# Kernel tuning notes

Hardware: AMD Instinct MI355X
Metric: run time of the kernel (lower is better)

## Reference

```python
import jax, jax.numpy as jnp
import numpy as np

NB = 8          # num_bins
HID = 128       # hidden channels of coupling ResidualNet
TB = 3.0        # tail_bound
MINB = 1e-3     # min bin width / height
MIND = 1e-3     # min derivative
DCONST = float(np.log(np.exp(1.0 - MIND) - 1.0))  # softplus(DCONST)+MIND == 1
LU_EPS = 1e-3


def rqs_inverse(x, uw, uh, ud):
    """Inverse monotonic rational-quadratic spline with linear tails (nflows math).
    x: [B,F]; uw,uh broadcastable to [B,F,NB]; ud broadcastable to [B,F,NB-1]."""
    K = NB
    uw = jnp.broadcast_to(uw, x.shape + (K,))
    uh = jnp.broadcast_to(uh, x.shape + (K,))
    ud = jnp.broadcast_to(ud, x.shape + (K - 1,))
    ud = jnp.pad(ud, [(0, 0)] * x.ndim + [(1, 1)], constant_values=DCONST)  # boundary derivs = 1
    inside = (x >= -TB) & (x <= TB)
    xi = jnp.clip(x, -TB, TB)

    def knots(u):
        v = MINB + (1.0 - MINB * K) * jax.nn.softmax(u, -1)
        c = jnp.concatenate([jnp.zeros(x.shape + (1,), x.dtype), jnp.cumsum(v, -1)], -1)
        c = 2.0 * TB * c - TB
        c = c.at[..., 0].set(-TB).at[..., -1].set(TB)
        return c, c[..., 1:] - c[..., :-1]

    cw, w = knots(uw)   # x-knots / bin widths
    ch, h = knots(uh)   # y-knots / bin heights
    d = MIND + jax.nn.softplus(ud)  # [B,F,K+1] knot derivatives

    # searchsorted on cumheights (inverse direction)
    locs = ch.at[..., -1].add(1e-6)
    idx = jnp.clip(jnp.sum((xi[..., None] >= locs).astype(jnp.int32), -1) - 1, 0, K - 1)[..., None]
    g = lambda a: jnp.take_along_axis(a, idx, -1)[..., 0]
    in_cw, in_w, in_ch, in_h = g(cw), g(w), g(ch), g(h)
    delta = in_h / in_w
    d0 = g(d)
    d1 = jnp.take_along_axis(d, idx + 1, -1)[..., 0]

    t = xi - in_ch
    s = d0 + d1 - 2.0 * delta
    a = t * s + in_h * (delta - d0)
    b = in_h * d0 - t * s
    c = -delta * t
    root = (2.0 * c) / (-b - jnp.sqrt(b * b - 4.0 * a * c))
    out = root * in_w + in_cw
    tm = root * (1.0 - root)
    den = delta + s * tm
    dnum = delta ** 2 * (d1 * root ** 2 + 2.0 * delta * tm + d0 * (1.0 - root) ** 2)
    ld = -(jnp.log(dnum) - 2.0 * jnp.log(den))
    return jnp.where(inside, out, x), jnp.where(inside, ld, 0.0)


def resnet(x, Wi, bi, Wb, bb, Wo, bo):
    # nflows ResidualNet: initial linear, 2 pre-activation residual blocks, final linear
    t = x @ Wi + bi
    for j in range(2):
        r = jax.nn.relu(t) @ Wb[2 * j] + bb[2 * j]
        r = jax.nn.relu(r) @ Wb[2 * j + 1] + bb[2 * j + 1]
        t = t + r
    return t @ Wo + bo


def coupling_inverse(z, Wi, bi, Wb, bb, Wo, bo, uw_u, uh_u, ud_u):
    # alternating mask: even dims = identity split, odd dims = transform split
    ident, trans = z[:, 0::2], z[:, 1::2]
    # unconditional spline on identity features is inverted FIRST, then feeds the net
    ident, ld_u = rqs_inverse(ident, uw_u, uh_u, ud_u)
    B, F = trans.shape
    p = resnet(ident, Wi, bi, Wb, bb, Wo, bo).reshape(B, F, 3 * NB - 1)
    scale = 1.0 / np.sqrt(HID)  # nflows divides widths/heights by sqrt(hidden_features)
    trans, ld_t = rqs_inverse(trans, p[..., :NB] * scale, p[..., NB:2 * NB] * scale, p[..., 2 * NB:])
    out = jnp.stack([ident, trans], -1).reshape(B, -1)
    return out, jnp.sum(ld_u, -1) + jnp.sum(ld_t, -1)


def log_prob(x, loc, log_scale, Wi, bi, Wb, bb, Wo, bo, uw_u, uh_u, ud_u,
             lu_lower, lu_upper, lu_ud, lu_b, perms):
    N, T, D = x.shape
    z = x.reshape(-1, D)
    lq = jnp.zeros((z.shape[0],), x.dtype)
    for i in (2, 1, 0):  # flows = [C0,LU0,C1,LU1,C2,LU2]; invert in reverse order
        # LULinearPermute.inverse: permute, then y = L(Ux) + b, logdet = sum log diag(U)
        zp = z[:, perms[i]]
        diag = jax.nn.softplus(lu_ud[i]) + LU_EPS
        U = jnp.triu(lu_upper[i], 1) + jnp.diag(diag)
        L = jnp.tril(lu_lower[i], -1) + jnp.eye(D, dtype=x.dtype)
        z = (zp @ U.T) @ L.T + lu_b[i]
        lq = lq + jnp.sum(jnp.log(diag))
        z, ld = coupling_inverse(z, Wi[i], bi[i], Wb[i], bb[i], Wo[i], bo[i],
                                 uw_u[i], uh_u[i], ud_u[i])
        lq = lq + ld
    # DiagGaussian base log-prob
    lq = lq - 0.5 * D * jnp.log(2.0 * jnp.pi) \
            - jnp.sum(log_scale + 0.5 * ((z - loc) / jnp.exp(log_scale)) ** 2, -1)
    return lq.reshape(N, T)


def setup_inputs():
    key = jax.random.key(0)
    ks = jax.random.split(key, 16)
    N, T, D, F = 8, 512, 550, 275
    OUT = F * (3 * NB - 1)
    s = 0.1
    return {
        "x": jax.random.normal(ks[0], (N, T, D), jnp.float32),
        "loc": 0.1 * jax.random.normal(ks[1], (D,), jnp.float32),
        "log_scale": jnp.zeros((D,), jnp.float32),
        "Wi": s * jax.random.normal(ks[2], (3, F, HID), jnp.float32),
        "bi": jnp.zeros((3, HID), jnp.float32),
        "Wb": s * jax.random.normal(ks[3], (3, 4, HID, HID), jnp.float32),
        "bb": jnp.zeros((3, 4, HID), jnp.float32),
        "Wo": 0.01 * jax.random.normal(ks[4], (3, HID, OUT), jnp.float32),
        "bo": 0.01 * jax.random.normal(ks[5], (3, OUT), jnp.float32),
        "uw_u": jax.random.uniform(ks[6], (3, F, NB), jnp.float32),
        "uh_u": jax.random.uniform(ks[7], (3, F, NB), jnp.float32),
        "ud_u": jax.random.uniform(ks[8], (3, F, NB - 1), jnp.float32),
        "lu_lower": 0.05 * jax.random.normal(ks[9], (3, D, D), jnp.float32),
        "lu_upper": 0.05 * jax.random.normal(ks[10], (3, D, D), jnp.float32),
        "lu_ud": jnp.full((3, D), DCONST, jnp.float32),
        "lu_b": jnp.zeros((3, D), jnp.float32),
        "perms": jnp.stack([jax.random.permutation(ks[11 + i], D) for i in range(3)]).astype(jnp.int32),
    }


def reference(x, loc, log_scale, Wi, bi, Wb, bb, Wo, bo, uw_u, uh_u, ud_u,
              lu_lower, lu_upper, lu_ud, lu_b, perms):
    # log_prob(x).reshape(N, T); calculate_likelihood would just apply exp/nan->0/clamp on top.
    return log_prob(x, loc, log_scale, Wi, bi, Wb, bb, Wo, bo, uw_u, uh_u, ud_u,
                    lu_lower, lu_upper, lu_ud, lu_b, perms)
```

## Files before the change

kernel.cpp:

```cpp
#include <hip/hip_runtime.h>


#define D_DIM 550
#define D_PAD 576
#define N_PAD_A 640
#define F_DIM 275
#define F_PAD 320
#define FP_HALF 288
#define HID_DIM 128
#define OUT_DIM 6325
#define OUT_PAD 6400
#define FT_PAD 276
#define WO2_ROWS (FT_PAD*32)
#define WO_GX (WO2_ROWS/64)
#define B_ROWS 4096
#define NBINS 8
#define TB_C 3.0f
#define MINB_C 0.001f
#define MIND_C 0.001f
#define DCONST_C 0.53974233f
#define LUEPS_C 0.001f
#define RSQRT_HID 0.08838834764831845f

typedef unsigned short ushort_t;
typedef __attribute__((ext_vector_type(8))) short short8;
typedef __attribute__((ext_vector_type(8))) unsigned short ushort8;
typedef __attribute__((ext_vector_type(4))) float f32x4;

__device__ __forceinline__ ushort_t f2bf(float f){
    union{float f; unsigned u;} v; v.f = f;
    unsigned r = v.u + 0x7fffu + ((v.u>>16)&1u);
    return (ushort_t)(r>>16);
}
__device__ __forceinline__ float bf2f(ushort_t h){
    union{unsigned u; float f;} v; v.u = ((unsigned)h)<<16;
    return v.f;
}
__device__ __forceinline__ float softplusf(float x){
    return fmaxf(x, 0.f) + __logf(1.f + __expf(-fabsf(x)));
}

__device__ __forceinline__ void knots_from_u(const float* u, float* c, float* w){
    float m = u[0];
#pragma unroll
    for(int k=1;k<NBINS;k++) m = fmaxf(m, u[k]);
    float e[NBINS]; float s = 0.f;
#pragma unroll
    for(int k=0;k<NBINS;k++){ e[k] = __expf(u[k]-m); s += e[k]; }
    float inv = 1.f/s;
    float cum = 0.f;
    c[0] = -TB_C;
#pragma unroll
    for(int k=0;k<NBINS;k++){
        float v = MINB_C + (1.f - MINB_C*(float)NBINS)*e[k]*inv;
        cum += v;
        c[k+1] = 2.f*TB_C*cum - TB_C;
    }
    c[NBINS] = TB_C;
#pragma unroll
    for(int k=0;k<NBINS;k++) w[k] = c[k+1]-c[k];
}

__device__ __forceinline__ void rqs_inv(float x,
                                        const float* cw, const float* w,
                                        const float* ch, const float* h,
                                        const float* d,
                                        float& out, float& ld){
    bool inside = (x >= -TB_C) && (x <= TB_C);
    float xi = fminf(fmaxf(x, -TB_C), TB_C);
    int idx = 0;
#pragma unroll
    for(int j=1;j<NBINS;j++) idx += (xi >= ch[j]) ? 1 : 0;
    float icw=cw[0], iw=w[0], ich=ch[0], ih=h[0], d0=d[0], d1=d[1];
#pragma unroll
    for(int j=1;j<NBINS;j++){
        if(idx==j){ icw=cw[j]; iw=w[j]; ich=ch[j]; ih=h[j]; d0=d[j]; d1=d[j+1]; }
    }
    float delta = ih/iw;
    float t  = xi - ich;
    float s  = d0 + d1 - 2.f*delta;
    float a  = t*s + ih*(delta - d0);
    float b  = ih*d0 - t*s;
    float c  = -delta*t;
    float disc = b*b - 4.f*a*c;
    float root = 2.f*c / (-b - sqrtf(fmaxf(disc, 0.f)));
    float o  = root*iw + icw;
    float tm = root*(1.f-root);
    float den  = delta + s*tm;
    float dnum = delta*delta*(d1*root*root + 2.f*delta*tm + d0*(1.f-root)*(1.f-root));
    float l = 2.f*__logf(den) - __logf(dnum);
    out = inside ? o : x;
    ld  = inside ? l : 0.f;
}


__global__ void build_knots_kernel(const float* __restrict__ uw_u,
                                   const float* __restrict__ uh_u,
                                   const float* __restrict__ ud_u,
                                   float* __restrict__ knots){
    int g = blockIdx.x*blockDim.x + threadIdx.x;
    if(g >= 3*F_DIM) return;
    float* kb = knots + (size_t)g*43;
    float c[9], w[8];
    knots_from_u(uw_u + (size_t)g*8, c, w);
#pragma unroll
    for(int k=0;k<9;k++) kb[k]=c[k];
#pragma unroll
    for(int k=0;k<8;k++) kb[9+k]=w[k];
    knots_from_u(uh_u + (size_t)g*8, c, w);
#pragma unroll
    for(int k=0;k<9;k++) kb[17+k]=c[k];
#pragma unroll
    for(int k=0;k<8;k++) kb[26+k]=w[k];
    float dend = MIND_C + softplusf(DCONST_C);
    kb[34]=dend; kb[42]=dend;
    const float* ud = ud_u + (size_t)g*7;
#pragma unroll
    for(int k=0;k<7;k++) kb[35+k] = MIND_C + softplusf(ud[k]);
}

__global__ void logdiag_kernel(const float* __restrict__ lu_ud, float* __restrict__ outv){
    int tid = threadIdx.x;
    float s = 0.f;
    for(int k=tid; k<3*D_DIM; k+=256) s += __logf(softplusf(lu_ud[k]) + LUEPS_C);
#pragma unroll
    for(int o=32;o>0;o>>=1) s += __shfl_down(s, o);
    __shared__ float sm[4];
    if((tid&63)==0) sm[tid>>6]=s;
    __syncthreads();
    if(tid==0) outv[0] = sm[0]+sm[1]+sm[2]+sm[3];
}

__global__ void build_L_bf16(const float* __restrict__ lower,
                             ushort_t* __restrict__ Lmb){
    int l = blockIdx.z;
    lower += (size_t)l*D_DIM*D_DIM;
    Lmb += (size_t)l*N_PAD_A*D_PAD;
    int k = blockIdx.x*blockDim.x + threadIdx.x;
    int j = blockIdx.y;
    if(k >= D_DIM) return;
    float lv = (j>k) ? lower[(size_t)j*D_DIM+k] : (j==k ? 1.f : 0.f);
    Lmb[(size_t)j*D_PAD+k] = f2bf(lv);
}

__global__ void build_UT_bf16(const float* __restrict__ upper,
                              const float* __restrict__ ud,
                              const int* __restrict__ perm,
                              ushort_t* __restrict__ UpTb){
    int l = blockIdx.z;
    upper += (size_t)l*D_DIM*D_DIM; ud += (size_t)l*D_DIM; perm += (size_t)l*D_DIM;
    UpTb += (size_t)l*N_PAD_A*D_PAD;
    __shared__ float t[32][33];
    int j0 = blockIdx.x*32, k0 = blockIdx.y*32;
    int tx = threadIdx.x, ty = threadIdx.y;
#pragma unroll
    for(int i=0;i<32;i+=8){
        int j = j0+ty+i, k = k0+tx;
        float uv = 0.f;
        if(j<D_DIM && k<D_DIM){
            if(j<k)       uv = upper[(size_t)j*D_DIM+k];
            else if(j==k) uv = softplusf(ud[k]) + LUEPS_C;
        }
        t[ty+i][tx] = uv;
    }
    __syncthreads();
#pragma unroll
    for(int i=0;i<32;i+=8){
        int k = k0+ty+i, j = j0+tx;
        if(k<D_DIM)
            UpTb[(size_t)perm[k]*D_PAD + j] = f2bf(t[tx][ty+i]);
    }
}

__global__ void convert_pad(const float* __restrict__ in, ushort_t* __restrict__ out,
                            int M, int K, int Mpad, int Kpad){
    int idx = blockIdx.x*256 + threadIdx.x;
    if(idx >= Mpad*Kpad) return;
    int r = idx / Kpad, c = idx - r*Kpad;
    float v = (r<M && c<K) ? in[(size_t)r*K+c] : 0.f;
    out[idx] = f2bf(v);
}

template<int REMAP>
__global__ void transpose_convert(const float* __restrict__ in, ushort_t* __restrict__ out,
                                  int K, int N, int Kpad, int Npad, long s_in, long s_out){
    in += (size_t)blockIdx.z*s_in; out += (size_t)blockIdx.z*s_out;
    __shared__ float t[32][33];
    int kb = blockIdx.x*32, nb = blockIdx.y*32;
    int tx = threadIdx.x, ty = threadIdx.y;
#pragma unroll
    for(int i=0;i<32;i+=8){
        int k = kb+ty+i, n = nb+tx;
        t[ty+i][tx] = (k<K && n<N) ? in[(size_t)k*N+n] : 0.f;
    }
    __syncthreads();
#pragma unroll
    for(int i=0;i<32;i+=8){
        int n = nb+ty+i, k = kb+tx;
        if(REMAP){
            if(n < OUT_DIM && k < Kpad){
                int f = n/23, j = n - 23*f;
                out[(size_t)(f*32+j)*Kpad+k] = f2bf(t[tx][ty+i]);
            }
        } else if(n<Npad && k<Kpad){
            out[(size_t)n*Kpad+k] = f2bf(t[tx][ty+i]);
        }
    }
}

__global__ void reorder_bias(const float* __restrict__ bo, float* __restrict__ bo2){
    int idx = blockIdx.x*256 + threadIdx.x;
    if(idx >= 3*OUT_DIM) return;
    int l = idx/OUT_DIM, n = idx%OUT_DIM;
    int f = n/23, j = n - 23*f;
    bo2[(size_t)l*WO2_ROWS + f*32 + j] = bo[idx];
}

template<int OUTBF>
__global__ __launch_bounds__(256)
void gemm_mfma(const ushort_t* __restrict__ A, const ushort_t* __restrict__ Bt,
               const float* __restrict__ bias, void* __restrict__ Cv,
               int M, int N, int Kpad, long sA, long sB, long sC){
    A  += (size_t)blockIdx.z*sA;
    Bt += (size_t)blockIdx.z*sB;
    __shared__ ushort_t As[128][72];
    __shared__ ushort_t Bs[128][72];
    int tid = threadIdx.x;
    int row0 = blockIdx.y*128, col0 = blockIdx.x*128;
    int wave = tid>>6, lane = tid&63;
    int wm = wave&1, wn = wave>>1;
    int lm = lane&15, quad = lane>>4;
    f32x4 acc[4][4] = {};
    for(int k0=0; k0<Kpad; k0+=64){
#pragma unroll
        for(int it=0; it<4; it++){
            int c = tid + it*256;
            int r = c>>3, c8 = (c&7)*8;
            *(ushort8*)&As[r][c8] = *(const ushort8*)(A + (size_t)(row0+r)*Kpad + k0 + c8);
            *(ushort8*)&Bs[r][c8] = *(const ushort8*)(Bt + (size_t)(col0+r)*Kpad + k0 + c8);
        }
        __syncthreads();
#pragma unroll
        for(int ks=0; ks<2; ks++){
            short8 af[4], bfr[4];
#pragma unroll
            for(int i=0;i<4;i++){
                af[i]  = *(const short8*)&As[wm*64 + i*16 + lm][ks*32 + quad*8];
                bfr[i] = *(const short8*)&Bs[wn*64 + i*16 + lm][ks*32 + quad*8];
            }
#pragma unroll
            for(int i=0;i<4;i++)
#pragma unroll
                for(int j=0;j<4;j++)
                    acc[i][j] = __builtin_amdgcn_mfma_f32_16x16x32_bf16(af[i], bfr[j], acc[i][j], 0, 0, 0);
        }
        __syncthreads();
    }
#pragma unroll
    for(int i=0;i<4;i++){
        int rbase = row0 + wm*64 + i*16 + quad*4;
#pragma unroll
        for(int j=0;j<4;j++){
            int gc = col0 + wn*64 + j*16 + lm;
            if(gc >= N) continue;
            float bv = bias[gc];
#pragma unroll
            for(int r=0;r<4;r++){
                int gr = rbase + r;
                float v = acc[i][j][r] + bv;
                if(OUTBF) ((ushort_t*)Cv + (size_t)blockIdx.z*sC)[(size_t)gr*N+gc] = f2bf(v);
                else      ((float*)Cv + (size_t)blockIdx.z*sC)[(size_t)gr*N+gc] = v;
            }
        }
    }
}

__global__ __launch_bounds__(256)
void resnet_fused(const ushort_t* __restrict__ identb,
                  const ushort_t* __restrict__ WiT,
                  const float* __restrict__ bi,
                  const ushort_t* __restrict__ WbT,
                  const float* __restrict__ bb,
                  ushort_t* __restrict__ tb){
    __shared__ ushort_t As2[16][136];
    int tid = threadIdx.x, wave = tid>>6, lane = tid&63;
    int lm = lane&15, quad = lane>>4;
    int r0 = blockIdx.x*16;
    int arow = r0 + lm;
    f32x4 cur[2] = {};
    f32x4 tsv[2];
    for(int k0=0; k0<F_PAD; k0+=64){
        const ushort_t* ap = identb + (size_t)arow*F_PAD + k0 + quad*8;
        short8 af0 = *(const short8*)(ap);
        short8 af1 = *(const short8*)(ap + 32);
#pragma unroll
        for(int jj=0;jj<2;jj++){
            int n = (wave*2+jj)*16 + lm;
            const ushort_t* wp = WiT + (size_t)n*F_PAD + k0 + quad*8;
            short8 b0 = *(const short8*)(wp);
            short8 b1 = *(const short8*)(wp + 32);
            cur[jj] = __builtin_amdgcn_mfma_f32_16x16x32_bf16(af0, b0, cur[jj], 0, 0, 0);
            cur[jj] = __builtin_amdgcn_mfma_f32_16x16x32_bf16(af1, b1, cur[jj], 0, 0, 0);
        }
    }
#pragma unroll
    for(int jj=0;jj<2;jj++){
        float bv = bi[(wave*2+jj)*16 + lm];
#pragma unroll
        for(int r=0;r<4;r++) cur[jj][r] += bv;
        tsv[jj] = cur[jj];
    }
    short8 wA[2][4], wB[2][4];
#pragma unroll
    for(int jj=0;jj<2;jj++){
        int n = (wave*2+jj)*16 + lm;
        const ushort_t* wp = WbT + (size_t)n*128 + quad*8;
#pragma unroll
        for(int ks=0;ks<4;ks++) wA[jj][ks] = *(const short8*)(wp + ks*32);
    }
#pragma unroll
    for(int st=0; st<4; st++){
        __syncthreads();
#pragma unroll
        for(int jj=0;jj<2;jj++)
#pragma unroll
            for(int r=0;r<4;r++)
                As2[quad*4 + r][(wave*2+jj)*16 + lm] = f2bf(fmaxf(cur[jj][r], 0.f));
        if(st < 3){
#pragma unroll
            for(int jj=0;jj<2;jj++){
                int n = (wave*2+jj)*16 + lm;
                const ushort_t* wp = WbT + (size_t)(st+1)*128*128 + (size_t)n*128 + quad*8;
#pragma unroll
                for(int ks=0;ks<4;ks++){
                    if(st & 1) wA[jj][ks] = *(const short8*)(wp + ks*32);
                    else       wB[jj][ks] = *(const short8*)(wp + ks*32);
                }
            }
        }
        __syncthreads();
        short8 af[4];
#pragma unroll
        for(int ks=0;ks<4;ks++) af[ks] = *(const short8*)&As2[lm][ks*32 + quad*8];
        f32x4 acc[2] = {};
#pragma unroll
        for(int ks=0;ks<4;ks++){
#pragma unroll
            for(int jj=0;jj<2;jj++){
                short8 bf = (st & 1) ? wB[jj][ks] : wA[jj][ks];
                acc[jj] = __builtin_amdgcn_mfma_f32_16x16x32_bf16(af[ks], bf, acc[jj], 0, 0, 0);
            }
        }
#pragma unroll
        for(int jj=0;jj<2;jj++){
            float bv = bb[st*128 + (wave*2+jj)*16 + lm];
#pragma unroll
            for(int r=0;r<4;r++) acc[jj][r] += bv;
        }
        if(st==1 || st==3){
#pragma unroll
            for(int jj=0;jj<2;jj++){
#pragma unroll
                for(int r=0;r<4;r++) acc[jj][r] += tsv[jj][r];
                tsv[jj] = acc[jj];
            }
        }
#pragma unroll
        for(int jj=0;jj<2;jj++) cur[jj] = acc[jj];
    }
#pragma unroll
    for(int jj=0;jj<2;jj++)
#pragma unroll
        for(int r=0;r<4;r++)
            tb[(size_t)(r0 + quad*4 + r)*HID_DIM + (wave*2+jj)*16 + lm] = f2bf(cur[jj][r]);
}

__global__ __launch_bounds__(256)
void zodd_transpose(const float* __restrict__ z2, float* __restrict__ z2oddT){
    __shared__ float s[32][65];
    int r0 = blockIdx.x*64, f0 = blockIdx.y*32;
    int tid = threadIdx.x;
    int f = tid & 31, rb = tid >> 5;
#pragma unroll
    for(int rr=0; rr<8; rr++){
        int r = rb + rr*8;
        int fg = f0 + f;
        float v = (fg < F_DIM) ? z2[(size_t)(r0+r)*D_DIM + 2*fg + 1] : 0.f;
        s[f][r] = v;
    }
    __syncthreads();
    int lane = tid & 63, fb = tid >> 6;
#pragma unroll
    for(int ff=0; ff<8; ff++){
        int fo = fb + ff*4;
        z2oddT[(size_t)(f0+fo)*B_ROWS + r0 + lane] = s[fo][lane];
    }
}

__global__ __launch_bounds__(256, 4)
void wo_spline(const ushort_t* __restrict__ tb,
               const ushort_t* __restrict__ Wo2,
               const float* __restrict__ bo2,
               const float* __restrict__ z2oddT,
               ushort_t* __restrict__ zOddT,
               float* __restrict__ ldpart){
    __shared__ __align__(16) char smem[128*67*4];
    __shared__ float ldred[128];
    ushort_t (*As)[72] = (ushort_t(*)[72])smem;
    ushort_t (*Bs)[72] = (ushort_t(*)[72])(smem + 128*72*2);
    float (*P)[67] = (float(*)[67])smem;
    int tid = threadIdx.x;
    int flat = blockIdx.y*WO_GX + blockIdx.x;
    int flat2 = (flat & 7)*(WO_GX*32/8) + (flat >> 3);
    int cbl = flat2 % WO_GX;
    int rbl = flat2 / WO_GX;
    int row0 = rbl*128, col0 = cbl*64;
    int wave = tid>>6, lane = tid&63;
    int wm = wave&1, wn = wave>>1;
    int lm = lane&15, quad = lane>>4;
    f32x4 acc[4][2] = {};
    for(int k0=0; k0<HID_DIM; k0+=64){
#pragma unroll
        for(int it=0; it<4; it++){
            int c = tid + it*256;
            int r = c>>3, c8 = (c&7)*8;
            *(ushort8*)&As[r][c8] = *(const ushort8*)(tb + (size_t)(row0+r)*HID_DIM + k0 + c8);
        }
#pragma unroll
        for(int it=0; it<2; it++){
            int v = tid + it*256;
            int n = v>>3, c8 = (v&7)*8;
            *(ushort8*)&Bs[n][c8] = *(const ushort8*)(Wo2 + (size_t)(col0+n)*HID_DIM + k0 + c8);
        }
        __syncthreads();
#pragma unroll
        for(int ks=0; ks<2; ks++){
            short8 af[4], bfr[2];
#pragma unroll
            for(int i=0;i<4;i++)
                af[i]  = *(const short8*)&As[wm*64 + i*16 + lm][ks*32 + quad*8];
#pragma unroll
            for(int j=0;j<2;j++)
                bfr[j] = *(const short8*)&Bs[wn*32 + j*16 + lm][ks*32 + quad*8];
#pragma unroll
            for(int i=0;i<4;i++)
#pragma unroll
                for(int j=0;j<2;j++)
                    acc[i][j] = __builtin_amdgcn_mfma_f32_16x16x32_bf16(af[i], bfr[j], acc[i][j], 0, 0, 0);
        }
        __syncthreads();
    }
#pragma unroll
    for(int j=0;j<2;j++){
        int cl = wn*32 + j*16 + lm;
        float bv = bo2[col0 + cl];
#pragma unroll
        for(int i=0;i<4;i++){
            int rl = wm*64 + i*16 + quad*4;
#pragma unroll
            for(int r=0;r<4;r++) P[rl+r][cl] = acc[i][j][r] + bv;
        }
    }
    __syncthreads();
    int row = tid & 127, feat = tid >> 7;
    int fg = cbl*2 + feat;
    float ldsum = 0.f;
    const float dend = MIND_C + softplusf(DCONST_C);
    if(fg < F_DIM){
        const float* q = &P[row][feat*32];
        float xv = z2oddT[(size_t)fg*B_ROWS + row0 + row];
        bool inside = (xv >= -TB_C) && (xv <= TB_C);
        float xi = fminf(fmaxf(xv, -TB_C), TB_C);
        float eh[8];
        float mh = -1e30f, sh = 0.f;
#pragma unroll
        for(int k=0;k<8;k++){ float u = q[8+k]*RSQRT_HID; eh[k]=u; mh=fmaxf(mh,u); }
#pragma unroll
        for(int k=0;k<8;k++){ eh[k] = __expf(eh[k]-mh); sh += eh[k]; }
        float invh = (1.f - MINB_C*8.f)/sh;
        int idx = 0;
        {
            float cum = 0.f;
#pragma unroll
            for(int k=0;k<7;k++){
                cum += MINB_C + eh[k]*invh;
                float ck = 2.f*TB_C*cum - TB_C;
                idx += (xi >= ck) ? 1 : 0;
            }
        }
        float ich = -TB_C, ihh = 0.f;
        {
            float cum = 0.f, cprev = -TB_C;
#pragma unroll
            for(int k=0;k<8;k++){
                cum += MINB_C + eh[k]*invh;
                float ck = (k==7) ? TB_C : (2.f*TB_C*cum - TB_C);
                if(idx==k){ ich = cprev; ihh = ck - cprev; }
                cprev = ck;
            }
        }
        float ew[8];
        float mw = -1e30f, sw = 0.f;
#pragma unroll
        for(int k=0;k<8;k++){ float u = q[k]*RSQRT_HID; ew[k]=u; mw=fmaxf(mw,u); }
#pragma unroll
        for(int k=0;k<8;k++){ ew[k] = __expf(ew[k]-mw); sw += ew[k]; }
        float invw = (1.f - MINB_C*8.f)/sw;
        float icw = -TB_C, iww = 0.f;
        {
            float cum = 0.f, cprev = -TB_C;
#pragma unroll
            for(int k=0;k<8;k++){
                cum += MINB_C + ew[k]*invw;
                float ck = (k==7) ? TB_C : (2.f*TB_C*cum - TB_C);
                if(idx==k){ icw = cprev; iww = ck - cprev; }
                cprev = ck;
            }
        }
        float d0 = (idx==0) ? dend : (MIND_C + softplusf(q[15+idx]));
        float d1 = (idx==7) ? dend : (MIND_C + softplusf(q[16+idx]));
        float delta = ihh/iww;
        float t  = xi - ich;
        float s  = d0 + d1 - 2.f*delta;
        float a  = t*s + ihh*(delta - d0);
        float b  = ihh*d0 - t*s;
        float c  = -delta*t;
        float disc = fmaxf(b*b - 4.f*a*c, 0.f);
        float root = 2.f*c / (-b - sqrtf(disc));
        float o  = root*iww + icw;
        float tm = root*(1.f-root);
        float den  = delta + s*tm;
        float dnum = delta*delta*(d1*root*root + 2.f*delta*tm + d0*(1.f-root)*(1.f-root));
        float l = 2.f*__logf(den) - __logf(dnum);
        zOddT[(size_t)fg*B_ROWS + row0 + row] = f2bf(inside ? o : xv);
        ldsum = inside ? l : 0.f;
    }
    if(tid >= 128) ldred[tid-128] = ldsum;
    __syncthreads();
    if(tid < 128) ldpart[(size_t)cbl*B_ROWS + row0 + tid] = ldsum + ldred[tid];
}

__global__ __launch_bounds__(256)
void interleave_z(const ushort_t* __restrict__ identb,
                  const ushort_t* __restrict__ zOddT,
                  const float* __restrict__ ldpart,
                  ushort_t* __restrict__ znb,
                  float* __restrict__ lq){
    __shared__ ushort_t s[FP_HALF][34];
    int r0 = blockIdx.x*32;
    int tid = threadIdx.x;
#pragma unroll
    for(int i=0;i<36;i++){
        int idx = tid + i*256;
        int f = idx>>5, r = idx&31;
        s[f][r] = zOddT[(size_t)f*B_ROWS + r0 + r];
    }
    __syncthreads();
    int wv = tid>>6, lane = tid&63;
#pragma unroll
    for(int k=0;k<8;k++){
        int r = wv + k*4;
        const ushort_t* idr = identb + (size_t)(r0+r)*F_PAD;
        unsigned* orow = (unsigned*)(znb + (size_t)(r0+r)*D_PAD);
#pragma unroll
        for(int c=0;c<5;c++){
            int f = lane + c*64;
            if(f < FP_HALF){
                unsigned lo = idr[f];
                unsigned hi = s[f][r];
                orow[f] = lo | (hi<<16);
            }
        }
    }
    if(tid < 32){
        float acc = 0.f;
        for(int cb=0; cb<WO_GX; cb++)
            acc += ldpart[(size_t)cb*B_ROWS + r0 + tid];
        lq[r0 + tid] += acc;
    }
}


__global__ __launch_bounds__(320)
void ident_spline_kernel(const float* __restrict__ z2, const float* __restrict__ knots,
                         int layer, ushort_t* __restrict__ identb,
                         float* __restrict__ lq){
    int row = blockIdx.x; int tid = threadIdx.x;
    float ldv = 0.f;
    if(tid < F_DIM){
        const float* kb = knots + ((size_t)(layer*F_DIM + tid))*43;
        float x = z2[(size_t)row*D_DIM + 2*tid];
        float o, l;
        rqs_inv(x, kb, kb+9, kb+17, kb+26, kb+34, o, l);
        identb[(size_t)row*F_PAD + tid] = f2bf(o);
        ldv = l;
    } else {
        identb[(size_t)row*F_PAD + tid] = 0;
    }
    __shared__ float sm[5];
    float v = ldv;
#pragma unroll
    for(int o=32;o>0;o>>=1) v += __shfl_down(v, o);
    if((tid&63)==0) sm[tid>>6]=v;
    __syncthreads();
    if(tid==0) lq[row] += sm[0]+sm[1]+sm[2]+sm[3]+sm[4];
}

__global__ __launch_bounds__(320)
void finalize_kernel(const ushort_t* __restrict__ zb, const float* __restrict__ loc,
                     const float* __restrict__ lsc, const float* __restrict__ lq,
                     const float* __restrict__ logdiag, float* __restrict__ out){
    int row = blockIdx.x; int tid = threadIdx.x;
    float s = 0.f;
    for(int k=tid; k<D_DIM; k+=320){
        float l = lsc[k];
        float diff = (bf2f(zb[(size_t)row*D_PAD+k])-loc[k])*__expf(-l);
        s += l + 0.5f*diff*diff;
    }
    __shared__ float sm[5];
#pragma unroll
    for(int o=32;o>0;o>>=1) s += __shfl_down(s, o);
    if((tid&63)==0) sm[tid>>6]=s;
    __syncthreads();
    if(tid==0){
        float tot = sm[0]+sm[1]+sm[2]+sm[3]+sm[4];
        out[row] = lq[row] + logdiag[0] - 275.f*1.8378770664f - tot;
    }
}


extern "C" void kernel_launch(void* const* d_in, const int* in_sizes, int n_in,
                              void* d_out, int out_size, void* d_ws, size_t ws_size,
                              hipStream_t stream){
    const float* x        = (const float*)d_in[0];
    const float* loc      = (const float*)d_in[1];
    const float* lsc      = (const float*)d_in[2];
    const float* Wi       = (const float*)d_in[3];
    const float* bi       = (const float*)d_in[4];
    const float* Wb       = (const float*)d_in[5];
    const float* bb       = (const float*)d_in[6];
    const float* Wo       = (const float*)d_in[7];
    const float* bo       = (const float*)d_in[8];
    const float* uw_u     = (const float*)d_in[9];
    const float* uh_u     = (const float*)d_in[10];
    const float* ud_u     = (const float*)d_in[11];
    const float* lu_lower = (const float*)d_in[12];
    const float* lu_upper = (const float*)d_in[13];
    const float* lu_ud    = (const float*)d_in[14];
    const float* lu_b     = (const float*)d_in[15];
    const int*   perms    = (const int*)d_in[16];
    float* out = (float*)d_out;

    char* base = (char*)d_ws;
    size_t off = 0;
    auto alloc = [&](size_t bytes)->char*{
        char* p = base + off;
        off += (bytes + 255) & ~(size_t)255;
        return p;
    };
    float* lq      = (float*)alloc(B_ROWS*4);
    float* zbias   = (float*)alloc(D_PAD*4);
    float* logdiag = (float*)alloc(64*4);
    float* knots   = (float*)alloc((size_t)3*F_DIM*43*4);
    float* z2      = (float*)alloc((size_t)B_ROWS*D_DIM*4);
    float* z2oddT  = (float*)alloc((size_t)FP_HALF*B_ROWS*4);
    float* ldpart  = (float*)alloc((size_t)WO_GX*B_ROWS*4);
    float* bo2     = (float*)alloc((size_t)3*WO2_ROWS*4);
    ushort_t* xb   = (ushort_t*)alloc((size_t)B_ROWS*D_PAD*2);
    ushort_t* zbf0 = (ushort_t*)alloc((size_t)B_ROWS*D_PAD*2);
    ushort_t* zbf1 = (ushort_t*)alloc((size_t)B_ROWS*D_PAD*2);
    ushort_t* zOddT= (ushort_t*)alloc((size_t)FP_HALF*B_ROWS*2);
    ushort_t* Lmb  = (ushort_t*)alloc((size_t)3*N_PAD_A*D_PAD*2);
    ushort_t* UpTb = (ushort_t*)alloc((size_t)3*N_PAD_A*D_PAD*2);
    ushort_t* Apb  = (ushort_t*)alloc((size_t)3*N_PAD_A*D_PAD*2);
    ushort_t* identb=(ushort_t*)alloc((size_t)B_ROWS*F_PAD*2);
    ushort_t* tb   = (ushort_t*)alloc((size_t)B_ROWS*HID_DIM*2);
    ushort_t* WiT  = (ushort_t*)alloc((size_t)3*HID_DIM*F_PAD*2);
    ushort_t* WbT  = (ushort_t*)alloc((size_t)3*4*HID_DIM*HID_DIM*2);
    ushort_t* Wo2  = (ushort_t*)alloc((size_t)3*WO2_ROWS*HID_DIM*2);

    hipMemsetAsync(lq, 0, B_ROWS*sizeof(float), stream);
    hipMemsetAsync(zbias, 0, D_PAD*sizeof(float), stream);
    hipMemsetAsync(zOddT, 0, (size_t)FP_HALF*B_ROWS*2, stream);
    hipMemsetAsync(Lmb, 0, (size_t)3*N_PAD_A*D_PAD*2, stream);
    hipMemsetAsync(UpTb, 0, (size_t)3*N_PAD_A*D_PAD*2, stream);
    hipMemsetAsync(Wo2, 0, (size_t)3*WO2_ROWS*HID_DIM*2, stream);
    hipMemsetAsync(bo2, 0, (size_t)3*WO2_ROWS*4, stream);
    build_knots_kernel<<<dim3((3*F_DIM+255)/256), dim3(256), 0, stream>>>(uw_u, uh_u, ud_u, knots);
    logdiag_kernel<<<dim3(1), dim3(256), 0, stream>>>(lu_ud, logdiag);
    convert_pad<<<dim3((B_ROWS*D_PAD+255)/256), dim3(256), 0, stream>>>(
        x, xb, B_ROWS, D_DIM, B_ROWS, D_PAD);
    build_L_bf16<<<dim3((D_DIM+255)/256, D_DIM, 3), dim3(256), 0, stream>>>(
        lu_lower, Lmb);
    dim3 tthr(32,8);
    build_UT_bf16<<<dim3(18, 18, 3), tthr, 0, stream>>>(
        lu_upper, lu_ud, perms, UpTb);
    gemm_mfma<1><<<dim3(5, 5, 3), dim3(256), 0, stream>>>(
        Lmb, UpTb, zbias, Apb, N_PAD_A, D_PAD, D_PAD,
        (long)N_PAD_A*D_PAD, (long)N_PAD_A*D_PAD, (long)N_PAD_A*D_PAD);
    transpose_convert<0><<<dim3(F_PAD/32, HID_DIM/32, 3), tthr, 0, stream>>>(
        Wi, WiT, F_DIM, HID_DIM, F_PAD, HID_DIM, (long)F_DIM*HID_DIM, (long)F_PAD*HID_DIM);
    transpose_convert<0><<<dim3(HID_DIM/32, HID_DIM/32, 12), tthr, 0, stream>>>(
        Wb, WbT, HID_DIM, HID_DIM, HID_DIM, HID_DIM, (long)HID_DIM*HID_DIM, (long)HID_DIM*HID_DIM);
    transpose_convert<1><<<dim3(HID_DIM/32, OUT_PAD/32, 3), tthr, 0, stream>>>(
        Wo, Wo2, HID_DIM, OUT_DIM, HID_DIM, OUT_PAD, (long)HID_DIM*OUT_DIM, (long)WO2_ROWS*HID_DIM);
    reorder_bias<<<dim3((3*OUT_DIM+255)/256), dim3(256), 0, stream>>>(bo, bo2);

    const ushort_t* zcur_b = xb;
    ushort_t* zbf[2] = {zbf0, zbf1};
    int zi = 0;

    for(int it=0; it<3; ++it){
        int i = 2 - it;

        gemm_mfma<0><<<dim3(N_PAD_A/128, B_ROWS/128), dim3(256), 0, stream>>>(
            zcur_b, Apb + (size_t)i*N_PAD_A*D_PAD, lu_b + (size_t)i*D_DIM,
            z2, B_ROWS, D_DIM, D_PAD, 0, 0, 0);

        zodd_transpose<<<dim3(B_ROWS/64, FP_HALF/32), dim3(256), 0, stream>>>(
            z2, z2oddT);

        ident_spline_kernel<<<dim3(B_ROWS), dim3(320), 0, stream>>>(
            z2, knots, i, identb, lq);

        resnet_fused<<<dim3(B_ROWS/16), dim3(256), 0, stream>>>(
            identb, WiT + (size_t)i*HID_DIM*F_PAD, bi + (size_t)i*HID_DIM,
            WbT + (size_t)i*4*HID_DIM*HID_DIM, bb + (size_t)i*4*HID_DIM, tb);

        wo_spline<<<dim3(WO_GX, B_ROWS/128), dim3(256), 0, stream>>>(
            tb, Wo2 + (size_t)i*WO2_ROWS*HID_DIM, bo2 + (size_t)i*WO2_ROWS,
            z2oddT, zOddT, ldpart);

        interleave_z<<<dim3(B_ROWS/32), dim3(256), 0, stream>>>(
            identb, zOddT, ldpart, zbf[zi], lq);

        zcur_b = zbf[zi];
        zi ^= 1;
    }

    finalize_kernel<<<dim3(B_ROWS), dim3(320), 0, stream>>>(
        zcur_b, loc, lsc, lq, logdiag, out);
}
```

Before: 418.8 us.

## Tighten Wo padding to 24 columns per feature, retile LU GEMM and transpose knots

Feature groups in the output projection are padded to 24 columns instead of 32, and wo_spline uses a 128x48 tile, so fewer MFMA columns are spent on padding and occupancy can rise to 6 blocks per CU. The per-layer LU apply GEMM gets a dedicated 64x128 tile kernel, which doubles the grid size so the CUs are better covered. Spline knot tables are stored transposed so that threads load them coalesced into registers. In exchange, each wo_spline block does less work, and the 48-column B tile leaves part of the load loop idle.

```diff
diff --git a/kernel.cpp b/kernel.cpp
--- a/kernel.cpp
+++ b/kernel.cpp
@@ -11,8 +11,9 @@
 #define OUT_DIM 6325
 #define OUT_PAD 6400
 #define FT_PAD 276
-#define WO2_ROWS (FT_PAD*32)
-#define WO_GX (WO2_ROWS/64)
+#define WO24_ROWS (FT_PAD*24)
+#define WO_GX (WO24_ROWS/48)
+#define KT_G (3*F_DIM)
 #define B_ROWS 4096
 #define NBINS 8
 #define TB_C 3.0f
@@ -97,26 +98,26 @@
 __global__ void build_knots_kernel(const float* __restrict__ uw_u,
                                    const float* __restrict__ uh_u,
                                    const float* __restrict__ ud_u,
-                                   float* __restrict__ knots){
+                                   float* __restrict__ kT){
     int g = blockIdx.x*blockDim.x + threadIdx.x;
-    if(g >= 3*F_DIM) return;
-    float* kb = knots + (size_t)g*43;
+    if(g >= KT_G) return;
     float c[9], w[8];
     knots_from_u(uw_u + (size_t)g*8, c, w);
 #pragma unroll
-    for(int k=0;k<9;k++) kb[k]=c[k];
-#pragma unroll
-    for(int k=0;k<8;k++) kb[9+k]=w[k];
+    for(int k=0;k<9;k++) kT[(size_t)k*KT_G + g] = c[k];
+#pragma unroll
+    for(int k=0;k<8;k++) kT[(size_t)(9+k)*KT_G + g] = w[k];
     knots_from_u(uh_u + (size_t)g*8, c, w);
 #pragma unroll
-    for(int k=0;k<9;k++) kb[17+k]=c[k];
-#pragma unroll
-    for(int k=0;k<8;k++) kb[26+k]=w[k];
+    for(int k=0;k<9;k++) kT[(size_t)(17+k)*KT_G + g] = c[k];
+#pragma unroll
+    for(int k=0;k<8;k++) kT[(size_t)(26+k)*KT_G + g] = w[k];
     float dend = MIND_C + softplusf(DCONST_C);
-    kb[34]=dend; kb[42]=dend;
+    kT[(size_t)34*KT_G + g] = dend;
+    kT[(size_t)42*KT_G + g] = dend;
     const float* ud = ud_u + (size_t)g*7;
 #pragma unroll
-    for(int k=0;k<7;k++) kb[35+k] = MIND_C + softplusf(ud[k]);
+    for(int k=0;k<7;k++) kT[(size_t)(35+k)*KT_G + g] = MIND_C + softplusf(ud[k]);
 }
 
 __global__ void logdiag_kernel(const float* __restrict__ lu_ud, float* __restrict__ outv){
@@ -200,7 +201,7 @@
         if(REMAP){
             if(n < OUT_DIM && k < Kpad){
                 int f = n/23, j = n - 23*f;
-                out[(size_t)(f*32+j)*Kpad+k] = f2bf(t[tx][ty+i]);
+                out[(size_t)(f*24+j)*Kpad+k] = f2bf(t[tx][ty+i]);
             }
         } else if(n<Npad && k<Kpad){
             out[(size_t)n*Kpad+k] = f2bf(t[tx][ty+i]);
@@ -213,7 +214,7 @@
     if(idx >= 3*OUT_DIM) return;
     int l = idx/OUT_DIM, n = idx%OUT_DIM;
     int f = n/23, j = n - 23*f;
-    bo2[(size_t)l*WO2_ROWS + f*32 + j] = bo[idx];
+    bo2[(size_t)l*WO24_ROWS + f*24 + j] = bo[idx];
 }
 
 template<int OUTBF>
@@ -271,6 +272,63 @@
                 if(OUTBF) ((ushort_t*)Cv + (size_t)blockIdx.z*sC)[(size_t)gr*N+gc] = f2bf(v);
                 else      ((float*)Cv + (size_t)blockIdx.z*sC)[(size_t)gr*N+gc] = v;
             }
+        }
+    }
+}
+
+__global__ __launch_bounds__(256, 4)
+void gemm_lu_apply(const ushort_t* __restrict__ A, const ushort_t* __restrict__ Bt,
+                   const float* __restrict__ bias, float* __restrict__ C){
+    __shared__ ushort_t As[64][72];
+    __shared__ ushort_t Bs[128][72];
+    int tid = threadIdx.x;
+    int row0 = blockIdx.y*64, col0 = blockIdx.x*128;
+    int wave = tid>>6, lane = tid&63;
+    int wm = wave&1, wn = wave>>1;
+    int lm = lane&15, quad = lane>>4;
+    f32x4 acc[2][4] = {};
+    for(int k0=0; k0<D_PAD; k0+=64){
+#pragma unroll
+        for(int it=0; it<2; it++){
+            int c = tid + it*256;
+            int r = c>>3, c8 = (c&7)*8;
+            *(ushort8*)&As[r][c8] = *(const ushort8*)(A + (size_t)(row0+r)*D_PAD + k0 + c8);
+        }
+#pragma unroll
+        for(int it=0; it<4; it++){
+            int c = tid + it*256;
+            int r = c>>3, c8 = (c&7)*8;
+            *(ushort8*)&Bs[r][c8] = *(const ushort8*)(Bt + (size_t)(col0+r)*D_PAD + k0 + c8);
+        }
+        __syncthreads();
+#pragma unroll
+        for(int ks=0; ks<2; ks++){
+            short8 af[2], bfr[4];
+#pragma unroll
+            for(int i=0;i<2;i++)
+                af[i]  = *(const short8*)&As[wm*32 + i*16 + lm][ks*32 + quad*8];
+#pragma unroll
+            for(int j=0;j<4;j++)
+                bfr[j] = *(const short8*)&Bs[wn*64 + j*16 + lm][ks*32 + quad*8];
+#pragma unroll
+            for(int i=0;i<2;i++)
+#pragma unroll
+                for(int j=0;j<4;j++)
+                    acc[i][j] = __builtin_amdgcn_mfma_f32_16x16x32_bf16(af[i], bfr[j], acc[i][j], 0, 0, 0);
+        }
+        __syncthreads();
+    }
+#pragma unroll
+    for(int i=0;i<2;i++){
+        int rbase = row0 + wm*32 + i*16 + quad*4;
+#pragma unroll
+        for(int j=0;j<4;j++){
+            int gc = col0 + wn*64 + j*16 + lm;
+            if(gc >= D_DIM) continue;
+            float bv = bias[gc];
+#pragma unroll
+            for(int r=0;r<4;r++)
+                C[(size_t)(rbase+r)*D_DIM+gc] = acc[i][j][r] + bv;
         }
     }
 }
@@ -397,28 +455,27 @@
     }
 }
 
-__global__ __launch_bounds__(256, 4)
+__global__ __launch_bounds__(256, 6)
 void wo_spline(const ushort_t* __restrict__ tb,
                const ushort_t* __restrict__ Wo2,
                const float* __restrict__ bo2,
                const float* __restrict__ z2oddT,
                ushort_t* __restrict__ zOddT,
                float* __restrict__ ldpart){
-    __shared__ __align__(16) char smem[128*67*4];
+    __shared__ __align__(16) char smem[128*51*4];
     __shared__ float ldred[128];
     ushort_t (*As)[72] = (ushort_t(*)[72])smem;
     ushort_t (*Bs)[72] = (ushort_t(*)[72])(smem + 128*72*2);
-    float (*P)[67] = (float(*)[67])smem;
+    float (*P)[51] = (float(*)[51])smem;
     int tid = threadIdx.x;
     int flat = blockIdx.y*WO_GX + blockIdx.x;
     int flat2 = (flat & 7)*(WO_GX*32/8) + (flat >> 3);
     int cbl = flat2 % WO_GX;
     int rbl = flat2 / WO_GX;
-    int row0 = rbl*128, col0 = cbl*64;
+    int row0 = rbl*128, col0 = cbl*48;
     int wave = tid>>6, lane = tid&63;
-    int wm = wave&1, wn = wave>>1;
     int lm = lane&15, quad = lane>>4;
-    f32x4 acc[4][2] = {};
+    f32x4 acc[2][3] = {};
     for(int k0=0; k0<HID_DIM; k0+=64){
 #pragma unroll
         for(int it=0; it<4; it++){
@@ -429,34 +486,36 @@
 #pragma unroll
         for(int it=0; it<2; it++){
             int v = tid + it*256;
-            int n = v>>3, c8 = (v&7)*8;
-            *(ushort8*)&Bs[n][c8] = *(const ushort8*)(Wo2 + (size_t)(col0+n)*HID_DIM + k0 + c8);
+            if(v < 384){
+                int n = v>>3, c8 = (v&7)*8;
+                *(ushort8*)&Bs[n][c8] = *(const ushort8*)(Wo2 + (size_t)(col0+n)*HID_DIM + k0 + c8);
+            }
         }
         __syncthreads();
 #pragma unroll
         for(int ks=0; ks<2; ks++){
-            short8 af[4], bfr[2];
-#pragma unroll
-            for(int i=0;i<4;i++)
-                af[i]  = *(const short8*)&As[wm*64 + i*16 + lm][ks*32 + quad*8];
-#pragma unroll
-            for(int j=0;j<2;j++)
-                bfr[j] = *(const short8*)&Bs[wn*32 + j*16 + lm][ks*32 + quad*8];
-#pragma unroll
-            for(int i=0;i<4;i++)
-#pragma unroll
-                for(int j=0;j<2;j++)
+            short8 af[2], bfr[3];
+#pragma unroll
+            for(int i=0;i<2;i++)
+                af[i]  = *(const short8*)&As[wave*32 + i*16 + lm][ks*32 + quad*8];
+#pragma unroll
+            for(int j=0;j<3;j++)
+                bfr[j] = *(const short8*)&Bs[j*16 + lm][ks*32 + quad*8];
+#pragma unroll
+            for(int i=0;i<2;i++)
+#pragma unroll
+                for(int j=0;j<3;j++)
                     acc[i][j] = __builtin_amdgcn_mfma_f32_16x16x32_bf16(af[i], bfr[j], acc[i][j], 0, 0, 0);
         }
         __syncthreads();
     }
 #pragma unroll
-    for(int j=0;j<2;j++){
-        int cl = wn*32 + j*16 + lm;
+    for(int j=0;j<3;j++){
+        int cl = j*16 + lm;
         float bv = bo2[col0 + cl];
 #pragma unroll
-        for(int i=0;i<4;i++){
-            int rl = wm*64 + i*16 + quad*4;
+        for(int i=0;i<2;i++){
+            int rl = wave*32 + i*16 + quad*4;
 #pragma unroll
             for(int r=0;r<4;r++) P[rl+r][cl] = acc[i][j][r] + bv;
         }
@@ -467,7 +526,7 @@
     float ldsum = 0.f;
     const float dend = MIND_C + softplusf(DCONST_C);
     if(fg < F_DIM){
-        const float* q = &P[row][feat*32];
+        const float* q = &P[row][feat*24];
         float xv = z2oddT[(size_t)fg*B_ROWS + row0 + row];
         bool inside = (xv >= -TB_C) && (xv <= TB_C);
         float xi = fminf(fmaxf(xv, -TB_C), TB_C);
@@ -582,16 +641,27 @@
 
 
 __global__ __launch_bounds__(320)
-void ident_spline_kernel(const float* __restrict__ z2, const float* __restrict__ knots,
+void ident_spline_kernel(const float* __restrict__ z2, const float* __restrict__ kTb,
                          int layer, ushort_t* __restrict__ identb,
                          float* __restrict__ lq){
     int row = blockIdx.x; int tid = threadIdx.x;
     float ldv = 0.f;
     if(tid < F_DIM){
-        const float* kb = knots + ((size_t)(layer*F_DIM + tid))*43;
+        const float* kT = kTb + (size_t)layer*F_DIM + tid;
+        float cw[9], w[8], ch[9], h[8], d[9];
+#pragma unroll
+        for(int k=0;k<9;k++) cw[k] = kT[(size_t)k*KT_G];
+#pragma unroll
+        for(int k=0;k<8;k++) w[k]  = kT[(size_t)(9+k)*KT_G];
+#pragma unroll
+        for(int k=0;k<9;k++) ch[k] = kT[(size_t)(17+k)*KT_G];
+#pragma unroll
+        for(int k=0;k<8;k++) h[k]  = kT[(size_t)(26+k)*KT_G];
+#pragma unroll
+        for(int k=0;k<9;k++) d[k]  = kT[(size_t)(34+k)*KT_G];
         float x = z2[(size_t)row*D_DIM + 2*tid];
         float o, l;
-        rqs_inv(x, kb, kb+9, kb+17, kb+26, kb+34, o, l);
+        rqs_inv(x, cw, w, ch, h, d, o, l);
         identb[(size_t)row*F_PAD + tid] = f2bf(o);
         ldv = l;
     } else {
@@ -661,11 +731,11 @@
     float* lq      = (float*)alloc(B_ROWS*4);
     float* zbias   = (float*)alloc(D_PAD*4);
     float* logdiag = (float*)alloc(64*4);
-    float* knots   = (float*)alloc((size_t)3*F_DIM*43*4);
+    float* knots   = (float*)alloc((size_t)43*KT_G*4);
     float* z2      = (float*)alloc((size_t)B_ROWS*D_DIM*4);
     float* z2oddT  = (float*)alloc((size_t)FP_HALF*B_ROWS*4);
     float* ldpart  = (float*)alloc((size_t)WO_GX*B_ROWS*4);
-    float* bo2     = (float*)alloc((size_t)3*WO2_ROWS*4);
+    float* bo2     = (float*)alloc((size_t)3*WO24_ROWS*4);
     ushort_t* xb   = (ushort_t*)alloc((size_t)B_ROWS*D_PAD*2);
     ushort_t* zbf0 = (ushort_t*)alloc((size_t)B_ROWS*D_PAD*2);
     ushort_t* zbf1 = (ushort_t*)alloc((size_t)B_ROWS*D_PAD*2);
@@ -677,16 +747,16 @@
     ushort_t* tb   = (ushort_t*)alloc((size_t)B_ROWS*HID_DIM*2);
     ushort_t* WiT  = (ushort_t*)alloc((size_t)3*HID_DIM*F_PAD*2);
     ushort_t* WbT  = (ushort_t*)alloc((size_t)3*4*HID_DIM*HID_DIM*2);
-    ushort_t* Wo2  = (ushort_t*)alloc((size_t)3*WO2_ROWS*HID_DIM*2);
+    ushort_t* Wo2  = (ushort_t*)alloc((size_t)3*WO24_ROWS*HID_DIM*2);
 
     hipMemsetAsync(lq, 0, B_ROWS*sizeof(float), stream);
     hipMemsetAsync(zbias, 0, D_PAD*sizeof(float), stream);
     hipMemsetAsync(zOddT, 0, (size_t)FP_HALF*B_ROWS*2, stream);
     hipMemsetAsync(Lmb, 0, (size_t)3*N_PAD_A*D_PAD*2, stream);
     hipMemsetAsync(UpTb, 0, (size_t)3*N_PAD_A*D_PAD*2, stream);
-    hipMemsetAsync(Wo2, 0, (size_t)3*WO2_ROWS*HID_DIM*2, stream);
-    hipMemsetAsync(bo2, 0, (size_t)3*WO2_ROWS*4, stream);
-    build_knots_kernel<<<dim3((3*F_DIM+255)/256), dim3(256), 0, stream>>>(uw_u, uh_u, ud_u, knots);
+    hipMemsetAsync(Wo2, 0, (size_t)3*WO24_ROWS*HID_DIM*2, stream);
+    hipMemsetAsync(bo2, 0, (size_t)3*WO24_ROWS*4, stream);
+    build_knots_kernel<<<dim3((KT_G+255)/256), dim3(256), 0, stream>>>(uw_u, uh_u, ud_u, knots);
     logdiag_kernel<<<dim3(1), dim3(256), 0, stream>>>(lu_ud, logdiag);
     convert_pad<<<dim3((B_ROWS*D_PAD+255)/256), dim3(256), 0, stream>>>(
         x, xb, B_ROWS, D_DIM, B_ROWS, D_PAD);
@@ -703,7 +773,7 @@
     transpose_convert<0><<<dim3(HID_DIM/32, HID_DIM/32, 12), tthr, 0, stream>>>(
         Wb, WbT, HID_DIM, HID_DIM, HID_DIM, HID_DIM, (long)HID_DIM*HID_DIM, (long)HID_DIM*HID_DIM);
     transpose_convert<1><<<dim3(HID_DIM/32, OUT_PAD/32, 3), tthr, 0, stream>>>(
-        Wo, Wo2, HID_DIM, OUT_DIM, HID_DIM, OUT_PAD, (long)HID_DIM*OUT_DIM, (long)WO2_ROWS*HID_DIM);
+        Wo, Wo2, HID_DIM, OUT_DIM, HID_DIM, OUT_PAD, (long)HID_DIM*OUT_DIM, (long)WO24_ROWS*HID_DIM);
     reorder_bias<<<dim3((3*OUT_DIM+255)/256), dim3(256), 0, stream>>>(bo, bo2);
 
     const ushort_t* zcur_b = xb;
@@ -713,9 +783,8 @@
     for(int it=0; it<3; ++it){
         int i = 2 - it;
 
-        gemm_mfma<0><<<dim3(N_PAD_A/128, B_ROWS/128), dim3(256), 0, stream>>>(
-            zcur_b, Apb + (size_t)i*N_PAD_A*D_PAD, lu_b + (size_t)i*D_DIM,
-            z2, B_ROWS, D_DIM, D_PAD, 0, 0, 0);
+        gemm_lu_apply<<<dim3(5, B_ROWS/64), dim3(256), 0, stream>>>(
+            zcur_b, Apb + (size_t)i*N_PAD_A*D_PAD, lu_b + (size_t)i*D_DIM, z2);
 
         zodd_transpose<<<dim3(B_ROWS/64, FP_HALF/32), dim3(256), 0, stream>>>(
             z2, z2oddT);
@@ -728,7 +797,7 @@
             WbT + (size_t)i*4*HID_DIM*HID_DIM, bb + (size_t)i*4*HID_DIM, tb);
 
         wo_spline<<<dim3(WO_GX, B_ROWS/128), dim3(256), 0, stream>>>(
-            tb, Wo2 + (size_t)i*WO2_ROWS*HID_DIM, bo2 + (size_t)i*WO2_ROWS,
+            tb, Wo2 + (size_t)i*WO24_ROWS*HID_DIM, bo2 + (size_t)i*WO24_ROWS,
             z2oddT, zOddT, ldpart);
 
         interleave_z<<<dim3(B_ROWS/32), dim3(256), 0, stream>>>(
```

Result: slower. 491.5 us (+17.4%).
